# Kernel optimization log

Measured on AMD Instinct MI355X. Metric: run time of the kernel, lower is better.

The kernel has to match this reference:

```python
import jax, jax.numpy as jnp
import numpy as np

NUM_EXPERTS = 8
TOP_K = 2
HIDDEN = 2048
INTER = 768


def setup_inputs() -> dict:
    key = jax.random.key(0)
    k0, k1, k2, k3, k4 = jax.random.split(key, 5)
    return {
        "hidden_states": jax.random.normal(k0, (2, 1024, HIDDEN), jnp.float32),
        "gate_w": jax.random.normal(k1, (NUM_EXPERTS, HIDDEN), jnp.float32) * 0.02,
        "w_gate": jax.random.normal(k2, (NUM_EXPERTS, HIDDEN, INTER), jnp.float32) * 0.02,
        "w_up": jax.random.normal(k3, (NUM_EXPERTS, HIDDEN, INTER), jnp.float32) * 0.02,
        "w_down": jax.random.normal(k4, (NUM_EXPERTS, INTER, HIDDEN), jnp.float32) * 0.02,
    }


def reference(hidden_states, gate_w, w_gate, w_up, w_down):
    B, S, H = hidden_states.shape
    x = hidden_states.reshape(-1, H)            # [T, H]
    T = x.shape[0]

    # Router: softmax in fp32, top-k, renormalize (norm_topk_prob=True)
    router_logits = jnp.einsum('td,ed->te', x, gate_w)          # [T, E]
    probs = jax.nn.softmax(router_logits.astype(jnp.float32), axis=-1)
    top_w, top_i = jax.lax.top_k(probs, TOP_K)                  # [T, K]
    top_w = top_w / jnp.sum(top_w, axis=-1, keepdims=True)
    top_w = top_w.astype(x.dtype)

    # Dense combine weights [T, E]: zero for unselected experts.
    # (top-k indices are distinct per token, so .set is exact.)
    w_dense = jnp.zeros((T, NUM_EXPERTS), x.dtype).at[
        jnp.arange(T)[:, None], top_i].set(top_w)

    # Per-expert SwiGLU MLP (Qwen3MoeMLP): down(silu(gate(x)) * up(x)).
    # EP dispatch/combine with ep_size=1 is an identity permutation, so the
    # math equals running every selected (token, expert) pair and combining.
    g = jax.nn.silu(jnp.einsum('td,edf->etf', x, w_gate))       # [E, T, F]
    u = jnp.einsum('td,edf->etf', x, w_up)                      # [E, T, F]
    y = jnp.einsum('etf,efd->etd', g * u, w_down)               # [E, T, H]

    out = jnp.einsum('etd,te->td', y, w_dense)                  # [T, H]
    return out.reshape(B, S, H), router_logits
```

## Files before the change

### kernel.cpp

```cpp
#include <hip/hip_runtime.h>
#include <hip/hip_bf16.h>
#include <math.h>

#define NTOK 2048
#define HID 2048
#define NEXP 8
#define FINT 768
#define TOPK 2

typedef __attribute__((ext_vector_type(8))) short bf16x8;
typedef __attribute__((ext_vector_type(4))) float f32x4;

static __device__ __forceinline__ unsigned short f2bf(float f) {
    union { float f; unsigned u; } v; v.f = f;
    unsigned r = v.u + 0x7fffu + ((v.u >> 16) & 1u);
    return (unsigned short)(r >> 16);
}

static __device__ __forceinline__ void gl16(const void* g, void* l) {
    __builtin_amdgcn_global_load_lds(
        (const __attribute__((address_space(1))) unsigned int*)g,
        (__attribute__((address_space(3))) unsigned int*)(uintptr_t)l,
        16, 0, 0);
}


static __device__ __forceinline__ void transpose_tile(
        const float* __restrict__ src, unsigned short* __restrict__ dst,
        int R, int C, int r0, int c0, float* tile, int tid) {
    {
        int rbase = tid >> 4;
        int ch = tid & 15;
        #pragma unroll
        for (int i = 0; i < 4; ++i) {
            int row = i * 16 + rbase;
            float4 v = *(const float4*)&src[(size_t)(r0 + row) * C + c0 + ch * 4];
            int p = ch ^ (row & 15);
            *(float4*)&tile[row * 64 + p * 4] = v;
        }
    }
    __syncthreads();
    {
        int r16 = (tid & 15) * 4;
        int cg = tid >> 4;
        float4 v[4];
        #pragma unroll
        for (int j = 0; j < 4; ++j) {
            int row = r16 + j;
            int p = cg ^ (row & 15);
            v[j] = *(const float4*)&tile[row * 64 + p * 4];
        }
        #pragma unroll
        for (int i = 0; i < 4; ++i) {
            float c0v = (i == 0) ? v[0].x : (i == 1) ? v[0].y : (i == 2) ? v[0].z : v[0].w;
            float c1v = (i == 0) ? v[1].x : (i == 1) ? v[1].y : (i == 2) ? v[1].z : v[1].w;
            float c2v = (i == 0) ? v[2].x : (i == 1) ? v[2].y : (i == 2) ? v[2].z : v[2].w;
            float c3v = (i == 0) ? v[3].x : (i == 1) ? v[3].y : (i == 2) ? v[3].z : v[3].w;
            ushort4 o = make_ushort4(f2bf(c0v), f2bf(c1v), f2bf(c2v), f2bf(c3v));
            *(uint2*)&dst[(size_t)(c0 + cg * 4 + i) * R + r0 + r16] = *(const uint2*)&o;
        }
    }
}

__global__ __launch_bounds__(256) void k1_router_wgwu(
        const float* __restrict__ x,
        const float* __restrict__ gw,
        const float* __restrict__ wg, const float* __restrict__ wu,
        float* __restrict__ out,
        float* __restrict__ logits_out,
        int* __restrict__ topk_idx,
        float* __restrict__ topk_w,
        unsigned short* __restrict__ xb,
        unsigned short* __restrict__ wgt, unsigned short* __restrict__ wut) {
    __shared__ __align__(16) float tile[64 * 64];
    int bid = blockIdx.x;
    if (bid < 512) {
        int w = threadIdx.x >> 6, l = threadIdx.x & 63;
        int t = bid * 4 + w;
        const float4* xr = (const float4*)(x + (size_t)t * HID);
        unsigned short* xbr = xb + (size_t)t * HID;
        float4 v[8];
        #pragma unroll
        for (int i = 0; i < 8; ++i) v[i] = xr[i * 64 + l];
        #pragma unroll
        for (int i = 0; i < 8; ++i)
            *(ushort4*)&xbr[(i * 64 + l) * 4] =
                make_ushort4(f2bf(v[i].x), f2bf(v[i].y), f2bf(v[i].z), f2bf(v[i].w));
        {
            float4 z = make_float4(0.f, 0.f, 0.f, 0.f);
            float4* orow = (float4*)(out + (size_t)t * HID);
            #pragma unroll
            for (int i = 0; i < 8; ++i) orow[i * 64 + l] = z;
        }
        float acc[NEXP];
        #pragma unroll
        for (int e = 0; e < NEXP; ++e) {
            const float4* gr = (const float4*)(gw + (size_t)e * HID);
            float a = 0.f;
            #pragma unroll
            for (int i = 0; i < 8; ++i) {
                float4 g = gr[i * 64 + l];
                a += v[i].x * g.x + v[i].y * g.y + v[i].z * g.z + v[i].w * g.w;
            }
            acc[e] = a;
        }
        #pragma unroll
        for (int off = 32; off > 0; off >>= 1)
            #pragma unroll
            for (int e = 0; e < NEXP; ++e) acc[e] += __shfl_xor(acc[e], off);
        if (l == 0) {
            float m = -1e30f;
            #pragma unroll
            for (int i = 0; i < NEXP; ++i) m = fmaxf(m, acc[i]);
            float p[NEXP];
            #pragma unroll
            for (int i = 0; i < NEXP; ++i) p[i] = expf(acc[i] - m);
            int i0 = 0;
            #pragma unroll
            for (int i = 1; i < NEXP; ++i) if (p[i] > p[i0]) i0 = i;
            int i1 = (i0 == 0) ? 1 : 0;
            #pragma unroll
            for (int i = 0; i < NEXP; ++i) if (i != i0 && p[i] > p[i1]) i1 = i;
            float w0 = p[i0], w1 = p[i1], sw = w0 + w1;
            topk_idx[t * 2 + 0] = i0;
            topk_idx[t * 2 + 1] = i1;
            topk_w[t * 2 + 0] = w0 / sw;
            topk_w[t * 2 + 1] = w1 / sw;
            #pragma unroll
            for (int i = 0; i < NEXP; ++i) logits_out[(size_t)t * NEXP + i] = acc[i];
        }
    } else {
        int idx = bid - 512;
        int e = idx / 768, sub = idx % 768;
        const float* src; unsigned short* dst;
        if (sub < 384) { src = wg; dst = wgt; }
        else           { src = wu; dst = wut; sub -= 384; }
        int tr = sub / 12, tc = sub % 12;
        src += (size_t)e * HID * FINT;
        dst += (size_t)e * HID * FINT;
        transpose_tile(src, dst, HID, FINT, tr * 64, tc * 64, tile, threadIdx.x);
    }
}

__global__ void moe_build_kernel(const int* __restrict__ topk_idx,
                                 const float* __restrict__ topk_w,
                                 int* __restrict__ counts,
                                 int* __restrict__ offsets,
                                 int* __restrict__ elist_t,
                                 float* __restrict__ elist_w,
                                 int* __restrict__ row_token,
                                 float* __restrict__ row_w) {
    __shared__ int scnt[NEXP];
    __shared__ int soff[NEXP];
    int tid = threadIdx.x;
    if (tid < NEXP) scnt[tid] = 0;
    __syncthreads();
    for (int t = tid; t < NTOK; t += 1024) {
        #pragma unroll
        for (int k = 0; k < TOPK; ++k) {
            int e = topk_idx[t * 2 + k];
            float w = topk_w[t * 2 + k];
            int slot = atomicAdd(&scnt[e], 1);
            elist_t[e * NTOK + slot] = t;
            elist_w[e * NTOK + slot] = w;
        }
    }
    __syncthreads();
    if (tid == 0) {
        int o = 0;
        for (int e = 0; e < NEXP; ++e) {
            soff[e] = o; offsets[e] = o; counts[e] = scnt[e]; o += scnt[e];
        }
    }
    __syncthreads();
    for (int e = 0; e < NEXP; ++e) {
        int c = scnt[e], o = soff[e];
        for (int s = tid; s < c; s += 1024) {
            row_token[o + s] = elist_t[e * NTOK + s];
            row_w[o + s]     = elist_w[e * NTOK + s];
        }
    }
}

__global__ __launch_bounds__(256) void k3_stagea_wd(
        const unsigned short* __restrict__ xb,
        const unsigned short* __restrict__ wgt,
        const unsigned short* __restrict__ wut,
        const float* __restrict__ wd,
        unsigned short* __restrict__ wdt,
        const int* __restrict__ counts,
        const int* __restrict__ offsets,
        const int* __restrict__ row_token,
        unsigned short* __restrict__ h_buf) {
    __shared__ __align__(16) char smem[49408];
    int bid = blockIdx.x;
    int tid = threadIdx.x;
    int idx = (int)(((bid >> 4) << 3) | (bid & 7));

    if (((bid >> 3) & 1) == 0) {
        int e = idx / 384, sub = idx % 384;
        int tr = sub / 32, tc = sub % 32;
        transpose_tile(wd + (size_t)e * FINT * HID,
                       wdt + (size_t)e * FINT * HID,
                       FINT, HID, tr * 64, tc * 64, (float*)smem, tid);
        return;
    }
    int e = idx & 7, mt = (idx >> 3) & 31, nt = idx >> 8;
    int count = counts[e];
    int m0 = mt * 64;
    if (m0 >= count) return;
    int off = offsets[e];
    int n0 = nt * 64;
    int mcnt = min(64, count - m0);

    char* AsB = smem;
    char* BgB = smem + 16384;
    char* BuB = smem + 32768;
    int* toks = (int*)(smem + 49152);
    if (tid < 64) toks[tid] = row_token[off + m0 + min(tid, mcnt - 1)];
    __syncthreads();

    int w = tid >> 6, l = tid & 63;
    int wr = w >> 1, wc = w & 1;
    int lr = l & 15, lh = l >> 4;
    int rA = w * 8 + (l >> 3);
    int cA = l & 7;

    const unsigned short* wgE = wgt + (size_t)e * FINT * HID + (size_t)n0 * HID;
    const unsigned short* wuE = wut + (size_t)e * FINT * HID + (size_t)n0 * HID;

    f32x4 gacc[2][2] = {};
    f32x4 uacc[2][2] = {};

    auto STAGE = [&](int buf, int k0) {
        #pragma unroll
        for (int i = 0; i < 2; ++i) {
            int row = 32 * i + rA;
            int sc = (cA ^ (row & 7)) << 3;
            size_t db = (size_t)buf * 8192 + (size_t)(32 * i + w * 8) * 128;
            gl16(xb + (size_t)toks[row] * HID + k0 + sc, AsB + db);
            gl16(wgE + (size_t)row * HID + k0 + sc,      BgB + db);
            gl16(wuE + (size_t)row * HID + k0 + sc,      BuB + db);
        }
    };

    auto COMPUTE = [&](int buf) {
        #pragma unroll
        for (int ks = 0; ks < 2; ++ks) {
            bf16x8 af[2], bg[2], bu[2];
            #pragma unroll
            for (int mi = 0; mi < 2; ++mi) {
                int row = wr * 32 + mi * 16 + lr;
                int byte = buf * 8192 + row * 128 + ((ks * 64 + lh * 16) ^ ((row & 7) << 4));
                af[mi] = *(const bf16x8*)(AsB + byte);
            }
            #pragma unroll
            for (int ni = 0; ni < 2; ++ni) {
                int row = wc * 32 + ni * 16 + lr;
                int byte = buf * 8192 + row * 128 + ((ks * 64 + lh * 16) ^ ((row & 7) << 4));
                bg[ni] = *(const bf16x8*)(BgB + byte);
                bu[ni] = *(const bf16x8*)(BuB + byte);
            }
            #pragma unroll
            for (int mi = 0; mi < 2; ++mi)
                #pragma unroll
                for (int ni = 0; ni < 2; ++ni) {
                    gacc[mi][ni] = __builtin_amdgcn_mfma_f32_16x16x32_bf16(af[mi], bg[ni], gacc[mi][ni], 0, 0, 0);
                    uacc[mi][ni] = __builtin_amdgcn_mfma_f32_16x16x32_bf16(af[mi], bu[ni], uacc[mi][ni], 0, 0, 0);
                }
        }
    };

    STAGE(0, 0);
    __syncthreads();
    for (int t = 0; t < HID / 64; ++t) {
        int cur = t & 1;
        if (t + 1 < HID / 64) STAGE(cur ^ 1, (t + 1) * 64);
        COMPUTE(cur);
        __syncthreads();
    }

    #pragma unroll
    for (int mi = 0; mi < 2; ++mi)
        #pragma unroll
        for (int ni = 0; ni < 2; ++ni)
            #pragma unroll
            for (int j = 0; j < 4; ++j) {
                int row = wr * 32 + mi * 16 + lh * 4 + j;
                if (row < mcnt) {
                    int col = wc * 32 + ni * 16 + lr;
                    float g = gacc[mi][ni][j], u = uacc[mi][ni][j];
                    float hv = g / (1.f + expf(-g)) * u;
                    h_buf[(size_t)(off + m0 + row) * FINT + n0 + col] = f2bf(hv);
                }
            }
}

__global__ __launch_bounds__(256) void moe_stage_b_mfma(
        const unsigned short* __restrict__ h_buf,
        const unsigned short* __restrict__ wdt,
        const int* __restrict__ counts,
        const int* __restrict__ offsets,
        const int* __restrict__ row_token,
        const float* __restrict__ row_w,
        float* __restrict__ out) {
    int e = blockIdx.x, mt = blockIdx.y, nt = blockIdx.z;
    int count = counts[e];
    int m0 = mt * 128;
    if (m0 >= count) return;
    int off = offsets[e];
    int n0 = nt * 128;
    int mcnt = min(128, count - m0);
    int tid = threadIdx.x;

    __shared__ __align__(16) unsigned short As[2][128 * 64];
    __shared__ __align__(16) unsigned short Bs[2][128 * 64];
    __shared__ int toks[128];
    __shared__ float rws[128];
    if (tid < 128) {
        int mm = min(tid, mcnt - 1);
        toks[tid] = row_token[off + m0 + mm];
        rws[tid] = row_w[off + m0 + mm];
    }
    __syncthreads();

    int w = tid >> 6, l = tid & 63;
    int wr = w >> 1, wc = w & 1;
    int lr = l & 15, lh = l >> 4;
    int wbase = (tid & 192) * 16;

    const unsigned short* hb = h_buf + (size_t)(off + m0) * FINT;
    const unsigned short* wdE = wdt + (size_t)e * HID * FINT + (size_t)n0 * FINT;

    f32x4 acc[4][4] = {};

    auto STAGE = [&](int buf, int k0) {
        #pragma unroll
        for (int i = 0; i < 4; ++i) {
            int s = i * 256 + tid;
            int row = s >> 3, c = s & 7;
            int sc = (c ^ (row & 7)) << 3;
            gl16(hb + (size_t)row * FINT + k0 + sc,  (char*)&As[buf][0] + i * 4096 + wbase);
            gl16(wdE + (size_t)row * FINT + k0 + sc, (char*)&Bs[buf][0] + i * 4096 + wbase);
        }
    };

    auto COMPUTE = [&](int buf) {
        #pragma unroll
        for (int ks = 0; ks < 2; ++ks) {
            bf16x8 af[4], bf[4];
            #pragma unroll
            for (int mi = 0; mi < 4; ++mi) {
                int row = wr * 64 + mi * 16 + lr;
                int byte = row * 128 + ((ks * 64 + lh * 16) ^ ((row & 7) << 4));
                af[mi] = *(const bf16x8*)((const char*)&As[buf][0] + byte);
            }
            #pragma unroll
            for (int ni = 0; ni < 4; ++ni) {
                int row = wc * 64 + ni * 16 + lr;
                int byte = row * 128 + ((ks * 64 + lh * 16) ^ ((row & 7) << 4));
                bf[ni] = *(const bf16x8*)((const char*)&Bs[buf][0] + byte);
            }
            #pragma unroll
            for (int mi = 0; mi < 4; ++mi)
                #pragma unroll
                for (int ni = 0; ni < 4; ++ni)
                    acc[mi][ni] = __builtin_amdgcn_mfma_f32_16x16x32_bf16(af[mi], bf[ni], acc[mi][ni], 0, 0, 0);
        }
    };

    STAGE(0, 0);
    __syncthreads();
    for (int t = 0; t < FINT / 64; ++t) {
        int cur = t & 1;
        if (t + 1 < FINT / 64) STAGE(cur ^ 1, (t + 1) * 64);
        COMPUTE(cur);
        __syncthreads();
    }

    #pragma unroll
    for (int mi = 0; mi < 4; ++mi)
        #pragma unroll
        for (int ni = 0; ni < 4; ++ni)
            #pragma unroll
            for (int j = 0; j < 4; ++j) {
                int row = wr * 64 + mi * 16 + lh * 4 + j;
                if (row < mcnt) {
                    int col = n0 + wc * 64 + ni * 16 + lr;
                    atomicAdd(&out[(size_t)toks[row] * HID + col],
                              rws[row] * acc[mi][ni][j]);
                }
            }
}

extern "C" void kernel_launch(void* const* d_in, const int* in_sizes, int n_in,
                              void* d_out, int out_size, void* d_ws, size_t ws_size,
                              hipStream_t stream) {
    const float* x       = (const float*)d_in[0];
    const float* gate_w  = (const float*)d_in[1];
    const float* w_gate  = (const float*)d_in[2];
    const float* w_up    = (const float*)d_in[3];
    const float* w_down  = (const float*)d_in[4];
    float* out = (float*)d_out;

    char* ws = (char*)d_ws;
    int*   topk_idx  = (int*)  (ws + 0);
    float* topk_w    = (float*)(ws + 16384);
    int*   counts    = (int*)  (ws + 32768);
    int*   offsets   = (int*)  (ws + 32800);
    int*   row_token = (int*)  (ws + 33024);
    float* row_w     = (float*)(ws + 49408);
    int*   elist_t   = (int*)  (ws + 65792);
    float* elist_w   = (float*)(ws + 131328);

    unsigned short* xb   = (unsigned short*)(ws + 196864);
    unsigned short* wg_t = (unsigned short*)(ws + 8585472);
    unsigned short* wu_t = (unsigned short*)(ws + 33751296);
    unsigned short* wd_t = (unsigned short*)(ws + 58917120);
    unsigned short* hb   = (unsigned short*)(ws + 84082944);

    float* logits_out = out + (size_t)NTOK * HID;

    k1_router_wgwu<<<512 + 6144, 256, 0, stream>>>(
        x, gate_w, w_gate, w_up, out, logits_out, topk_idx, topk_w, xb, wg_t, wu_t);
    moe_build_kernel<<<1, 1024, 0, stream>>>(topk_idx, topk_w, counts, offsets,
                                             elist_t, elist_w, row_token, row_w);
    k3_stagea_wd<<<3072 + 3072, 256, 0, stream>>>(
        xb, wg_t, wu_t, w_down, wd_t, counts, offsets, row_token, hb);
    dim3 gridB(NEXP, NTOK / 128, HID / 128);
    moe_stage_b_mfma<<<gridB, 256, 0, stream>>>(hb, wd_t, counts, offsets,
                                                row_token, row_w, out);
}
```

Before: 159.3 us.

## Fuse gate/up weight bf16 conversion into stage A GEMM loads

Stage A now reads the fp32 w_gate/w_up directly from global memory in registers, converts them to bf16 and writes them transposed into padded LDS tiles. This removes the separate pre-transpose pass and its bf16 workspace round trip. The w_down transpose moves into the router kernel. The cost is that each weight tile is reread and reconverted by every token tile (up to 32 m-tiles per expert), with fp32 loads doubling the bytes fetched per tile.

```diff
diff --git a/kernel.cpp b/kernel.cpp
--- a/kernel.cpp
+++ b/kernel.cpp
@@ -9,6 +9,7 @@
 #define TOPK 2
 
 typedef __attribute__((ext_vector_type(8))) short bf16x8;
+typedef __attribute__((ext_vector_type(4))) short bf16x4;
 typedef __attribute__((ext_vector_type(4))) float f32x4;
 
 static __device__ __forceinline__ unsigned short f2bf(float f) {
@@ -62,16 +63,16 @@
     }
 }
 
-__global__ __launch_bounds__(256) void k1_router_wgwu(
+__global__ __launch_bounds__(256) void k1_router_wd(
         const float* __restrict__ x,
         const float* __restrict__ gw,
-        const float* __restrict__ wg, const float* __restrict__ wu,
+        const float* __restrict__ wd,
         float* __restrict__ out,
         float* __restrict__ logits_out,
         int* __restrict__ topk_idx,
         float* __restrict__ topk_w,
         unsigned short* __restrict__ xb,
-        unsigned short* __restrict__ wgt, unsigned short* __restrict__ wut) {
+        unsigned short* __restrict__ wdt) {
     __shared__ __align__(16) float tile[64 * 64];
     int bid = blockIdx.x;
     if (bid < 512) {
@@ -131,14 +132,11 @@
         }
     } else {
         int idx = bid - 512;
-        int e = idx / 768, sub = idx % 768;
-        const float* src; unsigned short* dst;
-        if (sub < 384) { src = wg; dst = wgt; }
-        else           { src = wu; dst = wut; sub -= 384; }
-        int tr = sub / 12, tc = sub % 12;
-        src += (size_t)e * HID * FINT;
-        dst += (size_t)e * HID * FINT;
-        transpose_tile(src, dst, HID, FINT, tr * 64, tc * 64, tile, threadIdx.x);
+        int e = idx / 384, sub = idx % 384;
+        int tr = sub / 32, tc = sub % 32;
+        transpose_tile(wd + (size_t)e * FINT * HID,
+                       wdt + (size_t)e * FINT * HID,
+                       FINT, HID, tr * 64, tc * 64, tile, threadIdx.x);
     }
 }
 
@@ -182,41 +180,27 @@
     }
 }
 
-__global__ __launch_bounds__(256) void k3_stagea_wd(
+__global__ __launch_bounds__(256) void moe_stage_a2(
         const unsigned short* __restrict__ xb,
-        const unsigned short* __restrict__ wgt,
-        const unsigned short* __restrict__ wut,
-        const float* __restrict__ wd,
-        unsigned short* __restrict__ wdt,
+        const float* __restrict__ wg,
+        const float* __restrict__ wu,
         const int* __restrict__ counts,
         const int* __restrict__ offsets,
         const int* __restrict__ row_token,
         unsigned short* __restrict__ h_buf) {
-    __shared__ __align__(16) char smem[49408];
-    int bid = blockIdx.x;
-    int tid = threadIdx.x;
-    int idx = (int)(((bid >> 4) << 3) | (bid & 7));
-
-    if (((bid >> 3) & 1) == 0) {
-        int e = idx / 384, sub = idx % 384;
-        int tr = sub / 32, tc = sub % 32;
-        transpose_tile(wd + (size_t)e * FINT * HID,
-                       wdt + (size_t)e * FINT * HID,
-                       FINT, HID, tr * 64, tc * 64, (float*)smem, tid);
-        return;
-    }
-    int e = idx & 7, mt = (idx >> 3) & 31, nt = idx >> 8;
+    int e = blockIdx.x, mt = blockIdx.y, nt = blockIdx.z;
     int count = counts[e];
     int m0 = mt * 64;
     if (m0 >= count) return;
     int off = offsets[e];
     int n0 = nt * 64;
     int mcnt = min(64, count - m0);
-
-    char* AsB = smem;
-    char* BgB = smem + 16384;
-    char* BuB = smem + 32768;
-    int* toks = (int*)(smem + 49152);
+    int tid = threadIdx.x;
+
+    __shared__ __align__(16) unsigned short As[2][64 * 64];
+    __shared__ __align__(16) char BgR[2][64 * 136];
+    __shared__ __align__(16) char BuR[2][64 * 136];
+    __shared__ int toks[64];
     if (tid < 64) toks[tid] = row_token[off + m0 + min(tid, mcnt - 1)];
     __syncthreads();
 
@@ -225,58 +209,97 @@
     int lr = l & 15, lh = l >> 4;
     int rA = w * 8 + (l >> 3);
     int cA = l & 7;
-
-    const unsigned short* wgE = wgt + (size_t)e * FINT * HID + (size_t)n0 * HID;
-    const unsigned short* wuE = wut + (size_t)e * FINT * HID + (size_t)n0 * HID;
+    int kq = tid >> 4;
+    int nq = tid & 15;
+
+    const float* wgF = wg + (size_t)e * HID * FINT + n0;
+    const float* wuF = wu + (size_t)e * HID * FINT + n0;
 
     f32x4 gacc[2][2] = {};
     f32x4 uacc[2][2] = {};
-
-    auto STAGE = [&](int buf, int k0) {
+    float4 gld[4], uld[4];
+
+    auto LOADB = [&](int k0) {
+        #pragma unroll
+        for (int j = 0; j < 4; ++j) {
+            size_t ro = (size_t)(k0 + kq * 4 + j) * FINT + nq * 4;
+            gld[j] = *(const float4*)&wgF[ro];
+            uld[j] = *(const float4*)&wuF[ro];
+        }
+    };
+
+    auto WRITEB = [&](int buf) {
+        char* bg = &BgR[buf][0];
+        char* bu = &BuR[buf][0];
+        #define WB_(i, comp) { \
+            int r = nq * 4 + i; \
+            int byte = r * 136 + kq * 8; \
+            ushort4 og = make_ushort4(f2bf(gld[0].comp), f2bf(gld[1].comp), \
+                                      f2bf(gld[2].comp), f2bf(gld[3].comp)); \
+            ushort4 ou = make_ushort4(f2bf(uld[0].comp), f2bf(uld[1].comp), \
+                                      f2bf(uld[2].comp), f2bf(uld[3].comp)); \
+            *(uint2*)(bg + byte) = *(const uint2*)&og; \
+            *(uint2*)(bu + byte) = *(const uint2*)&ou; }
+        WB_(0, x) WB_(1, y) WB_(2, z) WB_(3, w)
+        #undef WB_
+    };
+
+    auto STAGEA = [&](int buf, int k0) {
         #pragma unroll
         for (int i = 0; i < 2; ++i) {
             int row = 32 * i + rA;
             int sc = (cA ^ (row & 7)) << 3;
-            size_t db = (size_t)buf * 8192 + (size_t)(32 * i + w * 8) * 128;
-            gl16(xb + (size_t)toks[row] * HID + k0 + sc, AsB + db);
-            gl16(wgE + (size_t)row * HID + k0 + sc,      BgB + db);
-            gl16(wuE + (size_t)row * HID + k0 + sc,      BuB + db);
+            size_t db = (size_t)(32 * i + w * 8) * 128;
+            gl16(xb + (size_t)toks[row] * HID + k0 + sc, (char*)&As[buf][0] + db);
         }
     };
 
     auto COMPUTE = [&](int buf) {
+        const char* bg = &BgR[buf][0];
+        const char* bu = &BuR[buf][0];
         #pragma unroll
         for (int ks = 0; ks < 2; ++ks) {
-            bf16x8 af[2], bg[2], bu[2];
+            bf16x8 af[2], bgf[2], buf_[2];
             #pragma unroll
             for (int mi = 0; mi < 2; ++mi) {
                 int row = wr * 32 + mi * 16 + lr;
-                int byte = buf * 8192 + row * 128 + ((ks * 64 + lh * 16) ^ ((row & 7) << 4));
-                af[mi] = *(const bf16x8*)(AsB + byte);
+                int byte = row * 128 + ((ks * 64 + lh * 16) ^ ((row & 7) << 4));
+                af[mi] = *(const bf16x8*)((const char*)&As[buf][0] + byte);
             }
             #pragma unroll
             for (int ni = 0; ni < 2; ++ni) {
                 int row = wc * 32 + ni * 16 + lr;
-                int byte = buf * 8192 + row * 128 + ((ks * 64 + lh * 16) ^ ((row & 7) << 4));
-                bg[ni] = *(const bf16x8*)(BgB + byte);
-                bu[ni] = *(const bf16x8*)(BuB + byte);
+                int byte = row * 136 + ks * 64 + lh * 16;
+                bf16x4 glo = *(const bf16x4*)(bg + byte);
+                bf16x4 ghi = *(const bf16x4*)(bg + byte + 8);
+                bf16x4 ulo = *(const bf16x4*)(bu + byte);
+                bf16x4 uhi = *(const bf16x4*)(bu + byte + 8);
+                bgf[ni] = __builtin_shufflevector(glo, ghi, 0, 1, 2, 3, 4, 5, 6, 7);
+                buf_[ni] = __builtin_shufflevector(ulo, uhi, 0, 1, 2, 3, 4, 5, 6, 7);
             }
             #pragma unroll
             for (int mi = 0; mi < 2; ++mi)
                 #pragma unroll
                 for (int ni = 0; ni < 2; ++ni) {
-                    gacc[mi][ni] = __builtin_amdgcn_mfma_f32_16x16x32_bf16(af[mi], bg[ni], gacc[mi][ni], 0, 0, 0);
-                    uacc[mi][ni] = __builtin_amdgcn_mfma_f32_16x16x32_bf16(af[mi], bu[ni], uacc[mi][ni], 0, 0, 0);
+                    gacc[mi][ni] = __builtin_amdgcn_mfma_f32_16x16x32_bf16(af[mi], bgf[ni], gacc[mi][ni], 0, 0, 0);
+                    uacc[mi][ni] = __builtin_amdgcn_mfma_f32_16x16x32_bf16(af[mi], buf_[ni], uacc[mi][ni], 0, 0, 0);
                 }
         }
     };
 
-    STAGE(0, 0);
-    __syncthreads();
-    for (int t = 0; t < HID / 64; ++t) {
+    LOADB(0);
+    STAGEA(0, 0);
+    WRITEB(0);
+    __syncthreads();
+    const int NT = HID / 64;
+    for (int t = 0; t < NT; ++t) {
         int cur = t & 1;
-        if (t + 1 < HID / 64) STAGE(cur ^ 1, (t + 1) * 64);
+        if (t + 1 < NT) {
+            LOADB((t + 1) * 64);
+            STAGEA(cur ^ 1, (t + 1) * 64);
+        }
         COMPUTE(cur);
+        if (t + 1 < NT) WRITEB(cur ^ 1);
         __syncthreads();
     }
 
@@ -414,19 +437,18 @@
     float* elist_w   = (float*)(ws + 131328);
 
     unsigned short* xb   = (unsigned short*)(ws + 196864);
-    unsigned short* wg_t = (unsigned short*)(ws + 8585472);
-    unsigned short* wu_t = (unsigned short*)(ws + 33751296);
     unsigned short* wd_t = (unsigned short*)(ws + 58917120);
     unsigned short* hb   = (unsigned short*)(ws + 84082944);
 
     float* logits_out = out + (size_t)NTOK * HID;
 
-    k1_router_wgwu<<<512 + 6144, 256, 0, stream>>>(
-        x, gate_w, w_gate, w_up, out, logits_out, topk_idx, topk_w, xb, wg_t, wu_t);
+    k1_router_wd<<<512 + 3072, 256, 0, stream>>>(
+        x, gate_w, w_down, out, logits_out, topk_idx, topk_w, xb, wd_t);
     moe_build_kernel<<<1, 1024, 0, stream>>>(topk_idx, topk_w, counts, offsets,
                                              elist_t, elist_w, row_token, row_w);
-    k3_stagea_wd<<<3072 + 3072, 256, 0, stream>>>(
-        xb, wg_t, wu_t, w_down, wd_t, counts, offsets, row_token, hb);
+    dim3 gridA(NEXP, NTOK / 64, FINT / 64);
+    moe_stage_a2<<<gridA, 256, 0, stream>>>(xb, w_gate, w_up, counts, offsets,
+                                            row_token, hb);
     dim3 gridB(NEXP, NTOK / 128, HID / 128);
     moe_stage_b_mfma<<<gridB, 256, 0, stream>>>(hb, wd_t, counts, offsets,
                                                 row_token, row_w, out);
```

Measured after the change: 178.8 us. 12.2% more time.
